# Kernel optimization log

Measured on AMD Instinct MI355X. Metric: run time of the kernel, lower is better.

Reference implementation:

```python
import jax, jax.numpy as jnp
import numpy as np

B, T, D = 32, 1024, 512
H = 1024          # hidden_size
LV = 128          # level_hidden_size
NREP = H // LV    # n_repeat = 8
NL = 2            # num_layers


def setup_inputs() -> dict:
    key = jax.random.key(0)
    ks = jax.random.split(key, 9)
    s = 0.02
    inp = {"x": jax.random.normal(ks[0], (B, T, D), jnp.float32)}
    # layer 0: input dim D; layer 1: input dim H
    inp["W_lstm0"] = jax.random.normal(ks[1], (4 * H, D + H), jnp.float32) * s
    inp["b_lstm0"] = jnp.zeros((4 * H,), jnp.float32)
    inp["W_lvl0"] = jax.random.normal(ks[2], (2 * LV, D + H), jnp.float32) * s
    inp["b_lvl0"] = jnp.zeros((2 * LV,), jnp.float32)
    inp["W_lstm1"] = jax.random.normal(ks[3], (4 * H, H + H), jnp.float32) * s
    inp["b_lstm1"] = jnp.zeros((4 * H,), jnp.float32)
    inp["W_lvl1"] = jax.random.normal(ks[4], (2 * LV, H + H), jnp.float32) * s
    inp["b_lvl1"] = jnp.zeros((2 * LV,), jnp.float32)
    return inp


def _cell(Wl, bl, Wv, bv, h, c, x_t):
    comb = jnp.concatenate([x_t, h], axis=-1)               # [B, in+H]
    gates = comb @ Wl.T + bl                                 # [B, 4H]
    cc_i, cc_f, cc_o, cc_g = jnp.split(gates, 4, axis=-1)
    lvl = comb @ Wv.T + bv                                   # [B, 2*LV]
    cc_i_h, cc_f_h = jnp.split(lvl, 2, axis=-1)
    i = jax.nn.sigmoid(cc_i)
    f = jax.nn.sigmoid(cc_f)
    o = jax.nn.sigmoid(cc_o)
    g = jnp.tanh(cc_g)
    p_f = jax.nn.softmax(cc_f_h, axis=-1)
    p_i = jax.nn.softmax(cc_i_h[..., ::-1], axis=-1)
    i_h = jnp.cumsum(p_f, axis=-1)                           # master input gate
    f_h = jnp.cumsum(p_i, axis=-1)[..., ::-1]                # master forget gate
    i_h = jnp.repeat(i_h, NREP, axis=-1)                     # [B, H]
    f_h = jnp.repeat(f_h, NREP, axis=-1)
    w = i_h * f_h
    c_new = w * (f * c + i * g) + (f_h - w) * c + (i_h - w) * g
    h_new = o * jnp.tanh(c_new)
    return h_new, c_new


def _run_layer(Wl, bl, Wv, bv, x):
    # x: [B, T, in]
    bsz = x.shape[0]
    h0 = jnp.zeros((bsz, H), x.dtype)
    c0 = jnp.zeros((bsz, H), x.dtype)

    def step(carry, x_t):
        h, c = carry
        h, c = _cell(Wl, bl, Wv, bv, h, c, x_t)
        return (h, c), h

    (_, _), hs = jax.lax.scan(step, (h0, c0), jnp.swapaxes(x, 0, 1))
    return jnp.swapaxes(hs, 0, 1)                            # [B, T, H]


def reference(x, W_lstm0, b_lstm0, W_lvl0, b_lvl0,
              W_lstm1, b_lstm1, W_lvl1, b_lvl1):
    out0 = _run_layer(W_lstm0, b_lstm0, W_lvl0, b_lvl0, x)
    out1 = _run_layer(W_lstm1, b_lstm1, W_lvl1, b_lvl1, out0)
    return out1
```

## Files before the change

### kernel.cpp

```cpp
#include <hip/hip_runtime.h>

namespace {
constexpr int kB  = 32;
constexpr int kT  = 1024;
constexpr int kD  = 512;
constexpr int kH  = 1024;
constexpr int kLV = 128;
constexpr int kNG = 4 * kH + 2 * kLV;
constexpr int kNBLK = 256;
constexpr int kNTHR = 512;
constexpr int kOffH0 = 16384;
constexpr int kRedOff = 3 * 1536 * 2 * 16;
constexpr int kIhOff  = kRedOff + 12288;
constexpr int kFhOff  = kIhOff + 512;
constexpr int kLdsBytes = kFhOff + 512;
}

typedef float vfloat4 __attribute__((ext_vector_type(4)));
typedef float floatx4 __attribute__((ext_vector_type(4)));
typedef _Float16 half8_t __attribute__((ext_vector_type(8)));
typedef unsigned short ushort_t;

static __device__ __forceinline__ unsigned ld_flag(const unsigned* p) {
  return __hip_atomic_load(p, __ATOMIC_RELAXED, __HIP_MEMORY_SCOPE_AGENT);
}
static __device__ __forceinline__ void st_flag(unsigned* p, unsigned v) {
  __hip_atomic_store(p, v, __ATOMIC_RELAXED, __HIP_MEMORY_SCOPE_AGENT);
}
static __device__ __forceinline__ float ld_coh(const float* p) {
  return __hip_atomic_load(p, __ATOMIC_RELAXED, __HIP_MEMORY_SCOPE_AGENT);
}
static __device__ __forceinline__ void st_wt(float* p, float v) {
  asm volatile("global_store_dword %0, %1, off sc0 sc1" :: "v"(p), "v"(v) : "memory");
}
static __device__ __forceinline__ void st_wtu(unsigned* p, unsigned v) {
  asm volatile("global_store_dword %0, %1, off sc0 sc1" :: "v"(p), "v"(v) : "memory");
}
static __device__ __forceinline__ void ld8h(uint4 v[8], const ushort_t* b) {
  asm volatile(
      "global_load_dwordx4 %0, %8, off sc0 sc1\n\t"
      "global_load_dwordx4 %1, %8, off offset:256 sc0 sc1\n\t"
      "global_load_dwordx4 %2, %8, off offset:512 sc0 sc1\n\t"
      "global_load_dwordx4 %3, %8, off offset:768 sc0 sc1\n\t"
      "global_load_dwordx4 %4, %8, off offset:1024 sc0 sc1\n\t"
      "global_load_dwordx4 %5, %8, off offset:1280 sc0 sc1\n\t"
      "global_load_dwordx4 %6, %8, off offset:1536 sc0 sc1\n\t"
      "global_load_dwordx4 %7, %8, off offset:1792 sc0 sc1\n\t"
      "s_waitcnt vmcnt(0)"
      : "=&v"(v[0]), "=&v"(v[1]), "=&v"(v[2]), "=&v"(v[3]),
        "=&v"(v[4]), "=&v"(v[5]), "=&v"(v[6]), "=&v"(v[7])
      : "v"(b)
      : "memory");
}
static __device__ __forceinline__ unsigned pkrtz(float a, float b) {
  return __builtin_bit_cast(unsigned, __builtin_amdgcn_cvt_pkrtz(a, b));
}
static __device__ __forceinline__ uint4 pack2(vfloat4 a, vfloat4 b) {
  uint4 r;
  r.x = pkrtz(a.x, a.y); r.y = pkrtz(a.z, a.w);
  r.z = pkrtz(b.x, b.y); r.w = pkrtz(b.z, b.w);
  return r;
}
static __device__ __forceinline__ floatx4 mfma16(uint4 a, uint4 b, floatx4 c) {
  return __builtin_amdgcn_mfma_f32_16x16x32_f16(
      __builtin_bit_cast(half8_t, a), __builtin_bit_cast(half8_t, b), c, 0, 0, 0);
}

__global__ __launch_bounds__(256) void cvt_fp16_kernel(
    const float* __restrict__ src, ushort_t* __restrict__ dst, int n8) {
  int i = blockIdx.x * 256 + threadIdx.x;
  if (i >= n8) return;
  const vfloat4* s4 = (const vfloat4*)src;
  vfloat4 a = s4[2 * i], b = s4[2 * i + 1];
  typedef _Float16 h8 __attribute__((ext_vector_type(8)));
  h8 o;
  o[0] = (_Float16)a.x; o[1] = (_Float16)a.y;
  o[2] = (_Float16)a.z; o[3] = (_Float16)a.w;
  o[4] = (_Float16)b.x; o[5] = (_Float16)b.y;
  o[6] = (_Float16)b.z; o[7] = (_Float16)b.w;
  ((h8*)dst)[i] = o;
}

__global__ __launch_bounds__(kNTHR, 2) void onlstm_kernel(
    const float* __restrict__ x,
    const float* __restrict__ bl0, const float* __restrict__ bv0,
    const float* __restrict__ bl1, const float* __restrict__ bv1,
    const ushort_t* __restrict__ wf0u, const ushort_t* __restrict__ wf1u,
    float* __restrict__ out, float* __restrict__ ws)
{
  const int tid = threadIdx.x;
  const int bid = blockIdx.x;

  unsigned* flagA  = (unsigned*)ws;
  unsigned* flagB  = (unsigned*)ws + 4096;
  unsigned* cflags = (unsigned*)ws + 8192;
  unsigned* cgenp  = (unsigned*)ws + 12288;
  ushort_t* h0f = (ushort_t*)(ws + kOffH0);
  ushort_t* h1f = h0f + 2 * kB * kH;
  float* gates0 = (float*)(h1f + 2 * kB * kH);
  float* gates1 = gates0 + kB * kNG;

  __shared__ __align__(16) char sb[kLdsBytes];
  uint4* wb4   = (uint4*)sb;
  float* redp  = (float*)(sb + kRedOff);
  float* ih_sh = (float*)(sb + kIhOff);
  float* fh_sh = (float*)(sb + kFhOff);

  auto signal = [&](unsigned* arr, unsigned v) {
    asm volatile("s_waitcnt vmcnt(0)" ::: "memory");
    __syncthreads();
    if (tid == 0) st_flag(&arr[bid * 16], v);
  };
  auto wait_ge = [&](unsigned* arr, int lo, int n, int tgt) {
    if (tid < n) {
      while ((int)(ld_flag(&arr[(lo + tid) * 16]) - (unsigned)tgt) < 0)
        __builtin_amdgcn_s_sleep(1);
    }
    __syncthreads();
    asm volatile("" ::: "memory");
  };
  unsigned iseq = 0;
  auto initbar = [&]() {
    ++iseq;
    asm volatile("s_waitcnt vmcnt(0)" ::: "memory");
    __syncthreads();
    if (bid == 0) {
      if (tid >= 1 && tid < kNBLK) {
        while (ld_flag(&cflags[tid * 16]) != iseq) __builtin_amdgcn_s_sleep(2);
      }
      __syncthreads();
      if (tid == 0) st_flag(cgenp, iseq);
    } else {
      if (tid == 0) {
        st_flag(&cflags[bid * 16], iseq);
        while (ld_flag(cgenp) != iseq) __builtin_amdgcn_s_sleep(2);
      }
      __syncthreads();
    }
    asm volatile("" ::: "memory");
  };

  int L, ntile, cb0;
  if (bid < 32)       { L = 0; ntile = 3; cb0 = bid * 48; }
  else if (bid < 120) { L = 0; ntile = 2; cb0 = 1536 + (bid - 32) * 32; }
  else                { L = 1; ntile = 2; cb0 = (bid - 120) * 32; }
  const int K   = L ? 2048 : 1536;
  const int ts4 = K * 2;
  const bool three = (ntile == 3);
  const int rstride = three ? 3 : 2;
  const ushort_t* wf = L ? wf1u : wf0u;
  const float* blp = L ? bl1 : bl0;
  const float* bvp = L ? bv1 : bv0;
  float* gatesL = L ? gates1 : gates0;

  const int lane = tid & 63;
  const int rt   = (tid >> 6) & 1;
  const int str  = tid >> 7;
  const int r_   = rt * 16 + (lane & 15);
  const int koct = lane >> 4;
  const int colg0 = cb0 + (lane & 15);
  const int colg1 = cb0 + 16 + (lane & 15);
  const int colg2 = cb0 + 32 + (lane & 15);

  auto redsl = [&](int slot, int accIdx) -> float* {
    return &redp[(((slot * 2 + rt) * rstride) + accIdx) * 256 + lane * 4];
  };

  for (int tt = 0; tt < ntile; ++tt) {
    const int colb = cb0 + tt * 16;
    for (int idx = tid; idx < ts4; idx += kNTHR) {
      int m = idx >> 6, l2 = idx & 63;
      size_t off = (size_t)(colb + (l2 & 15)) * K + m * 32 + 8 * (l2 >> 4);
      wb4[tt * ts4 + idx] = *(const uint4*)(wf + off);
    }
  }
  const float b0w = (colg0 < 4096) ? blp[colg0] : bvp[colg0 - 4096];
  const float b1w = (colg1 < 4096) ? blp[colg1] : bvp[colg1 - 4096];
  const float b2w = three ? ((colg2 < 4096) ? blp[colg2] : bvp[colg2 - 4096]) : 0.f;
  __syncthreads();

  if (tid == 0) { st_flag(&flagA[bid * 16], 0u); st_flag(&flagB[bid * 16], 0u); }
  { int idx = bid * kNTHR + tid;
    if (idx < 65536) st_wtu((unsigned*)h0f + idx, 0u); }
  float creg = 0.f;
  initbar();
  initbar();

  const int pbB  = (bid & 127) >> 2;
  const int qq4B = bid & 3;
  auto cellB = [&](const float* gbase, ushort_t* hb, float& cr, float* outp, int t) {
    const float* gr = gbase + (size_t)pbB * kNG;
    const bool cl = tid < 256;
    float vi = 0.f, vf = 0.f, vo = 0.f, vg = 0.f;
    int j = qq4B * 256 + tid;
    if (cl) {
      vi = ld_coh(gr + j);
      vf = ld_coh(gr + kH + j);
      vo = ld_coh(gr + 2 * kH + j);
      vg = ld_coh(gr + 3 * kH + j);
    }
    if (tid < 64) {
      float a0i = ld_coh(gr + 4096 + 2 * tid);
      float a1i = ld_coh(gr + 4096 + 2 * tid + 1);
      float a0f = ld_coh(gr + 4096 + kLV + 2 * tid);
      float a1f = ld_coh(gr + 4096 + kLV + 2 * tid + 1);
      float mi = fmaxf(a0i, a1i), mf = fmaxf(a0f, a1f);
#pragma unroll
      for (int d = 32; d > 0; d >>= 1) {
        mi = fmaxf(mi, __shfl_xor(mi, d));
        mf = fmaxf(mf, __shfl_xor(mf, d));
      }
      float e0i = __expf(a0i - mi), e1i = __expf(a1i - mi);
      float e0f = __expf(a0f - mf), e1f = __expf(a1f - mf);
      float si2 = e0i + e1i, sf2 = e0f + e1f;
      float Pi = si2, Pf = sf2;
#pragma unroll
      for (int d = 1; d < 64; d <<= 1) {
        float ni = __shfl_up(Pi, d);
        float nf = __shfl_up(Pf, d);
        if (tid >= d) { Pi += ni; Pf += nf; }
      }
      float Si = __shfl(Pi, 63), Sf = __shfl(Pf, 63);
      float pri = Pi - si2, prf = Pf - sf2;
      ih_sh[2 * tid]     = (prf + e0f) / Sf;
      ih_sh[2 * tid + 1] = (prf + e0f + e1f) / Sf;
      fh_sh[2 * tid]     = (Si - pri) / Si;
      fh_sh[2 * tid + 1] = (Si - pri - e0i) / Si;
    }
    __syncthreads();
    if (cl) {
      float i_ = 1.f / (1.f + __expf(-vi));
      float f_ = 1.f / (1.f + __expf(-vf));
      float o_ = 1.f / (1.f + __expf(-vo));
      float g_ = tanhf(vg);
      int l2 = j >> 3;
      float ih = ih_sh[l2], fh = fh_sh[l2];
      float w  = ih * fh;
      float cold = cr;
      float cn = w * (f_ * cold + i_ * g_) + (fh - w) * cold + (ih - w) * g_;
      float hn = o_ * tanhf(cn);
      cr = cn;
      float hnn = __shfl_xor(hn, 1);
      if (!(tid & 1))
        st_wtu((unsigned*)hb + ((size_t)pbB * kH + j) / 2, pkrtz(hn, hnn));
      if (outp) st_wt(outp + ((size_t)pbB * kT + t) * kH + j, hn);
    }
  };

  for (int e = 0; e <= kT; ++e) {
    const bool actA = L ? (e >= 1) : (e < kT);
    const size_t wpar = (size_t)(e & 1) * kB * kH;
    const size_t rpar = (size_t)((e + 1) & 1) * kB * kH;

    if (actA) {
      floatx4 a0 = {0.f,0.f,0.f,0.f}, a1 = a0, a2 = a0;
      if (L == 0) {
        const float* bx = x + ((size_t)r_ * kT + e) * kD + str * 32 + koct * 8;
        vfloat4 vx[8];
#pragma unroll
        for (int j = 0; j < 4; ++j) {
          vx[2*j]   = *(const vfloat4*)(bx + j * 128);
          vx[2*j+1] = *(const vfloat4*)(bx + j * 128 + 4);
        }
        uint4 pa[4];
#pragma unroll
        for (int j = 0; j < 4; ++j) pa[j] = pack2(vx[2*j], vx[2*j+1]);
#pragma unroll
        for (int j = 0; j < 4; ++j) {
          const int m = str + 4 * j;
          a0 = mfma16(pa[j], wb4[m * 64 + lane], a0);
          a1 = mfma16(pa[j], wb4[ts4 + m * 64 + lane], a1);
          if (three) a2 = mfma16(pa[j], wb4[2 * ts4 + m * 64 + lane], a2);
        }
        if (e > 0) wait_ge(flagB, 0, 128, e + 1);
        uint4 ph[8];
        ld8h(ph, h0f + rpar + (size_t)r_ * kH + str * 32 + koct * 8);
#pragma unroll
        for (int j = 0; j < 8; ++j) {
          const int m = 16 + str + 4 * j;
          a0 = mfma16(ph[j], wb4[m * 64 + lane], a0);
          a1 = mfma16(ph[j], wb4[ts4 + m * 64 + lane], a1);
          if (three) a2 = mfma16(ph[j], wb4[2 * ts4 + m * 64 + lane], a2);
        }
      } else {
        wait_ge(flagB, 0, 128, e + 1);
        uint4 pa[8];
        ld8h(pa, h0f + rpar + (size_t)r_ * kH + str * 32 + koct * 8);
#pragma unroll
        for (int j = 0; j < 8; ++j) {
          const int m = str + 4 * j;
          a0 = mfma16(pa[j], wb4[m * 64 + lane], a0);
          a1 = mfma16(pa[j], wb4[ts4 + m * 64 + lane], a1);
        }
        wait_ge(flagB, 128, 128, e + 1);
        uint4 pb[8];
        ld8h(pb, h1f + rpar + (size_t)r_ * kH + str * 32 + koct * 8);
#pragma unroll
        for (int j = 0; j < 8; ++j) {
          const int m = 32 + str + 4 * j;
          a0 = mfma16(pb[j], wb4[m * 64 + lane], a0);
          a1 = mfma16(pb[j], wb4[ts4 + m * 64 + lane], a1);
        }
      }
      if (!three) {
        if (str != 0) {
          *(floatx4*)redsl(str - 1, 0) = a0;
          *(floatx4*)redsl(str - 1, 1) = a1;
        }
        __syncthreads();
        if (str == 0) {
#pragma unroll
          for (int s2 = 0; s2 < 3; ++s2) {
            a0 += *(const floatx4*)redsl(s2, 0);
            a1 += *(const floatx4*)redsl(s2, 1);
          }
        }
      } else {
        if (str == 1 || str == 2) {
          *(floatx4*)redsl(str - 1, 0) = a0;
          *(floatx4*)redsl(str - 1, 1) = a1;
          *(floatx4*)redsl(str - 1, 2) = a2;
        }
        __syncthreads();
        if (str == 0) {
#pragma unroll
          for (int s2 = 0; s2 < 2; ++s2) {
            a0 += *(const floatx4*)redsl(s2, 0);
            a1 += *(const floatx4*)redsl(s2, 1);
            a2 += *(const floatx4*)redsl(s2, 2);
          }
        }
        __syncthreads();
        if (str == 3) {
          *(floatx4*)redsl(0, 0) = a0;
          *(floatx4*)redsl(0, 1) = a1;
          *(floatx4*)redsl(0, 2) = a2;
        }
        __syncthreads();
        if (str == 0) {
          a0 += *(const floatx4*)redsl(0, 0);
          a1 += *(const floatx4*)redsl(0, 1);
          a2 += *(const floatx4*)redsl(0, 2);
        }
      }
      if (str == 0) {
        const int rb = rt * 16 + koct * 4;
#pragma unroll
        for (int r = 0; r < 4; ++r)
          st_wt(gatesL + (size_t)(rb + r) * kNG + colg0, a0[r] + b0w);
#pragma unroll
        for (int r = 0; r < 4; ++r)
          st_wt(gatesL + (size_t)(rb + r) * kNG + colg1, a1[r] + b1w);
        if (three) {
#pragma unroll
          for (int r = 0; r < 4; ++r)
            st_wt(gatesL + (size_t)(rb + r) * kNG + colg2, a2[r] + b2w);
        }
      }
    }
    signal(flagA, (unsigned)(e + 1));

    if (bid < 128) {
      if (e < kT) {
        if (tid < 256) {
          int tgt = (tid < 120) ? e + 1 : e;
          while ((int)(ld_flag(&flagA[tid * 16]) - (unsigned)tgt) < 0)
            __builtin_amdgcn_s_sleep(1);
        }
        __syncthreads();
        asm volatile("" ::: "memory");
        cellB(gates0, h0f + wpar, creg, nullptr, e);
      }
    } else {
      if (e >= 1) {
        wait_ge(flagA, 120, 136, e + 1);
        cellB(gates1, h1f + wpar, creg, out, e - 1);
      }
    }
    signal(flagB, (unsigned)(e + 2));
  }
}

extern "C" void kernel_launch(void* const* d_in, const int* in_sizes, int n_in,
                              void* d_out, int out_size, void* d_ws, size_t ws_size,
                              hipStream_t stream) {
  const float* x   = (const float*)d_in[0];
  const float* Wl0 = (const float*)d_in[1];
  const float* bl0 = (const float*)d_in[2];
  const float* Wv0 = (const float*)d_in[3];
  const float* bv0 = (const float*)d_in[4];
  const float* Wl1 = (const float*)d_in[5];
  const float* bl1 = (const float*)d_in[6];
  const float* Wv1 = (const float*)d_in[7];
  const float* bv1 = (const float*)d_in[8];
  (void)in_sizes; (void)n_in; (void)out_size; (void)ws_size;

  float* ws = (float*)d_ws;
  const size_t kOffWFf = (size_t)kOffH0 + 32768 + 32768 + 2 * (size_t)kB * kNG;
  ushort_t* wf0 = (ushort_t*)(ws + kOffWFf);
  ushort_t* wf1 = wf0 + (size_t)4352 * 1536;

  {
    int n;
    n = 4096 * 1536 / 8;
    cvt_fp16_kernel<<<(n + 255) / 256, 256, 0, stream>>>(Wl0, wf0, n);
    n = 256 * 1536 / 8;
    cvt_fp16_kernel<<<(n + 255) / 256, 256, 0, stream>>>(
        Wv0, wf0 + (size_t)4096 * 1536, n);
    n = 4096 * 2048 / 8;
    cvt_fp16_kernel<<<(n + 255) / 256, 256, 0, stream>>>(Wl1, wf1, n);
    n = 256 * 2048 / 8;
    cvt_fp16_kernel<<<(n + 255) / 256, 256, 0, stream>>>(
        Wv1, wf1 + (size_t)4096 * 2048, n);
  }

  onlstm_kernel<<<dim3(kNBLK), dim3(kNTHR), 0, stream>>>(
      x, bl0, bv0, bl1, bv1, wf0, wf1, (float*)d_out, ws);
}
```

Baseline: 9.864 ms.

## Narrow inter-block flag waits to true producers and drop sleep in spins

Each cell block now waits only on the GEMM blocks whose gate columns it actually reads (hotB), and accepts the previous step for the rest. The h-row waits are done per wavefront, with no block barrier, and only on the flags that wavefront needs. The s_sleep backoff is removed from the spin loops and the output store becomes a plain store. The aim is to cut cross-block synchronisation latency on the per-timestep critical path. The cost is heavier polling traffic on the flags and subtle correctness risk if the dependency sets are wrong.

```diff
diff --git a/kernel.cpp b/kernel.cpp
--- a/kernel.cpp
+++ b/kernel.cpp
@@ -106,17 +106,18 @@
   float* ih_sh = (float*)(sb + kIhOff);
   float* fh_sh = (float*)(sb + kFhOff);
 
+  const int lane = tid & 63;
+  const int rt   = (tid >> 6) & 1;
+  const int str  = tid >> 7;
+
   auto signal = [&](unsigned* arr, unsigned v) {
     asm volatile("s_waitcnt vmcnt(0)" ::: "memory");
     __syncthreads();
     if (tid == 0) st_flag(&arr[bid * 16], v);
   };
-  auto wait_ge = [&](unsigned* arr, int lo, int n, int tgt) {
-    if (tid < n) {
-      while ((int)(ld_flag(&arr[(lo + tid) * 16]) - (unsigned)tgt) < 0)
-        __builtin_amdgcn_s_sleep(1);
-    }
-    __syncthreads();
+  auto wait_rows = [&](unsigned* arr, int baseBlk, int tgt) {
+    const int idx = baseBlk + rt * 64 + lane;
+    while ((int)(ld_flag(&arr[idx * 16]) - (unsigned)tgt) < 0) {}
     asm volatile("" ::: "memory");
   };
   unsigned iseq = 0;
@@ -153,9 +154,6 @@
   const float* bvp = L ? bv1 : bv0;
   float* gatesL = L ? gates1 : gates0;
 
-  const int lane = tid & 63;
-  const int rt   = (tid >> 6) & 1;
-  const int str  = tid >> 7;
   const int r_   = rt * 16 + (lane & 15);
   const int koct = lane >> 4;
   const int colg0 = cb0 + (lane & 15);
@@ -165,6 +163,33 @@
   auto redsl = [&](int slot, int accIdx) -> float* {
     return &redp[(((slot * 2 + rt) * rstride) + accIdx) * 256 + lane * 4];
   };
+
+  const int pbB  = (bid & 127) >> 2;
+  const int qq4B = bid & 3;
+  bool hotB = false;
+  if (bid < 128) {
+    if (tid < 120) {
+      int cb = tid < 32 ? tid * 48 : 1536 + (tid - 32) * 32;
+      int sp = tid < 32 ? 48 : 32;
+#pragma unroll
+      for (int q = 0; q < 4; ++q) {
+        int a = q * 1024 + qq4B * 256;
+        hotB = hotB || (cb < a + 256 && cb + sp > a);
+      }
+      hotB = hotB || (cb + sp > 4096);
+    }
+  } else {
+    if (tid < 136) {
+      int cb = tid * 32;
+      int a = qq4B * 256;
+#pragma unroll
+      for (int q = 0; q < 4; ++q) {
+        int aa = q * 1024 + a;
+        hotB = hotB || (cb < aa + 256 && cb + 32 > aa);
+      }
+      hotB = hotB || (cb + 32 > 4096);
+    }
+  }
 
   for (int tt = 0; tt < ntile; ++tt) {
     const int colb = cb0 + tt * 16;
@@ -186,8 +211,6 @@
   initbar();
   initbar();
 
-  const int pbB  = (bid & 127) >> 2;
-  const int qq4B = bid & 3;
   auto cellB = [&](const float* gbase, ushort_t* hb, float& cr, float* outp, int t) {
     const float* gr = gbase + (size_t)pbB * kNG;
     const bool cl = tid < 256;
@@ -243,7 +266,7 @@
       float hnn = __shfl_xor(hn, 1);
       if (!(tid & 1))
         st_wtu((unsigned*)hb + ((size_t)pbB * kH + j) / 2, pkrtz(hn, hnn));
-      if (outp) st_wt(outp + ((size_t)pbB * kT + t) * kH + j, hn);
+      if (outp) outp[((size_t)pbB * kT + t) * kH + j] = hn;
     }
   };
 
@@ -272,7 +295,7 @@
           a1 = mfma16(pa[j], wb4[ts4 + m * 64 + lane], a1);
           if (three) a2 = mfma16(pa[j], wb4[2 * ts4 + m * 64 + lane], a2);
         }
-        if (e > 0) wait_ge(flagB, 0, 128, e + 1);
+        if (e > 0) wait_rows(flagB, 0, e + 1);
         uint4 ph[8];
         ld8h(ph, h0f + rpar + (size_t)r_ * kH + str * 32 + koct * 8);
 #pragma unroll
@@ -283,7 +306,7 @@
           if (three) a2 = mfma16(ph[j], wb4[2 * ts4 + m * 64 + lane], a2);
         }
       } else {
-        wait_ge(flagB, 0, 128, e + 1);
+        wait_rows(flagB, 0, e + 1);
         uint4 pa[8];
         ld8h(pa, h0f + rpar + (size_t)r_ * kH + str * 32 + koct * 8);
 #pragma unroll
@@ -292,7 +315,7 @@
           a0 = mfma16(pa[j], wb4[m * 64 + lane], a0);
           a1 = mfma16(pa[j], wb4[ts4 + m * 64 + lane], a1);
         }
-        wait_ge(flagB, 128, 128, e + 1);
+        wait_rows(flagB, 128, e + 1);
         uint4 pb[8];
         ld8h(pb, h1f + rpar + (size_t)r_ * kH + str * 32 + koct * 8);
 #pragma unroll
@@ -363,9 +386,8 @@
     if (bid < 128) {
       if (e < kT) {
         if (tid < 256) {
-          int tgt = (tid < 120) ? e + 1 : e;
-          while ((int)(ld_flag(&flagA[tid * 16]) - (unsigned)tgt) < 0)
-            __builtin_amdgcn_s_sleep(1);
+          int tgt = hotB ? e + 1 : e;
+          while ((int)(ld_flag(&flagA[tid * 16]) - (unsigned)tgt) < 0) {}
         }
         __syncthreads();
         asm volatile("" ::: "memory");
@@ -373,7 +395,12 @@
       }
     } else {
       if (e >= 1) {
-        wait_ge(flagA, 120, 136, e + 1);
+        if (tid < 136) {
+          int tgt = hotB ? e + 1 : e;
+          while ((int)(ld_flag(&flagA[(120 + tid) * 16]) - (unsigned)tgt) < 0) {}
+        }
+        __syncthreads();
+        asm volatile("" ::: "memory");
         cellB(gates1, h1f + wpar, creg, out, e - 1);
       }
     }
```

Measured after the change: 9.606 ms. -2.6%, faster.
